# Kernel optimization log

Hardware: AMD Instinct MI355X
Metric: run time of the kernel (lower is better)

Reference implementation:

```python
import jax, jax.numpy as jnp
import numpy as np

N_NODES = 100000
N_EDGES = 1200000
IN_F = 64
OUT_F = 64


def setup_inputs() -> dict:
    key = jax.random.key(0)
    ks = jax.random.split(key, 8)
    rows = jax.random.randint(ks[0], (N_EDGES,), 0, N_NODES)
    cols = jax.random.randint(ks[1], (N_EDGES,), 0, N_NODES)
    vals = jax.random.uniform(ks[2], (N_EDGES,), dtype=jnp.float32)
    features = jax.random.normal(ks[3], (N_NODES, IN_F), dtype=jnp.float32)
    W1 = jax.random.normal(ks[4], (IN_F, OUT_F), dtype=jnp.float32) / np.sqrt(IN_F)
    b1 = jax.random.normal(ks[5], (OUT_F,), dtype=jnp.float32) * 0.01
    W2 = jax.random.normal(ks[6], (IN_F, OUT_F), dtype=jnp.float32) / np.sqrt(IN_F)
    b2 = jax.random.normal(ks[7], (OUT_F,), dtype=jnp.float32) * 0.01
    return {"rows": rows, "cols": cols, "vals": vals, "features": features,
            "W1": W1, "b1": b1, "W2": W2, "b2": b2}


def _spmm(rows, cols, vals, x):
    # y[r] = sum_{e: rows[e]==r} vals[e] * x[cols[e]]  -- COO SpMM via gather + segment_sum
    msgs = vals[:, None] * x[cols]  # [E, F]
    return jax.ops.segment_sum(msgs, rows, num_segments=N_NODES)


def reference(rows, cols, vals, features, W1, b1, W2, b2):
    # L1 = laplacian + selfLoop(identity)  =>  L1 @ X = L @ X + X
    agg1 = _spmm(rows, cols, vals, features) + features          # [N, inF]
    inter_feature = features * features                           # elementwise square
    agg2 = _spmm(rows, cols, vals, inter_feature)                 # [N, inF]
    part1 = agg1 @ W1 + b1                                        # linear
    part2 = agg2 @ W2 + b2                                        # interActTransform
    return part1 + part2
```

## Files before the change

kernel.cpp:

```cpp
#include <hip/hip_runtime.h>


#define ROWS_PER_BUCKET 128
#define ROW_SHIFT 7
#define NBUCK_PAD 784
#define SCAN_T 196
#define CAP 2048
#define CHUNK 4096
#define MAXB 2048
#define COL_BITS 17
#define COL_MASK 0x1FFFF
#define OVF_CAP 65536

typedef __attribute__((ext_vector_type(8))) short bf16x8;
typedef __attribute__((ext_vector_type(4))) float f32x4;

__device__ __forceinline__ unsigned short f2bf(float x) {
    unsigned u = __float_as_uint(x);
    unsigned r = (u + 0x7FFFu + ((u >> 16) & 1u)) >> 16;
    return (unsigned short)r;
}
__device__ __forceinline__ float bf2f(unsigned short h) {
    return __uint_as_float(((unsigned)h) << 16);
}

__global__ __launch_bounds__(256) void node_transform(
    const float* __restrict__ X, const float* __restrict__ W1,
    const float* __restrict__ b1, const float* __restrict__ W2,
    const float* __restrict__ b2, unsigned short* __restrict__ Yb,
    float* __restrict__ Z, int n_nodes)
{
    const int tid = threadIdx.x;
    const int lane = tid & 63;
    const int wave = tid >> 6;
    const int lg = lane >> 4;
    const int lr = lane & 15;

    const int base = blockIdx.x * 128 + wave * 32;

    bf16x8 bw1[2][4];
    bf16x8 bw2[2][4];
#pragma unroll
    for (int ks = 0; ks < 2; ++ks) {
#pragma unroll
        for (int cf = 0; cf < 4; ++cf) {
            const int col = cf * 16 + lr;
            const int k0 = ks * 32 + lg * 8;
            bf16x8 t1, t2;
#pragma unroll
            for (int j = 0; j < 8; ++j) {
                t1[j] = (short)f2bf(W1[(k0 + j) * 64 + col]);
                t2[j] = (short)f2bf(W2[(k0 + j) * 64 + col]);
            }
            bw1[ks][cf] = t1;
            bw2[ks][cf] = t2;
        }
    }

    f32x4 acc1[2][4];
    f32x4 acc2[2][4];
#pragma unroll
    for (int rf = 0; rf < 2; ++rf)
#pragma unroll
        for (int cf = 0; cf < 4; ++cf) {
            acc1[rf][cf] = (f32x4){0.f, 0.f, 0.f, 0.f};
            acc2[rf][cf] = (f32x4){0.f, 0.f, 0.f, 0.f};
        }

#pragma unroll
    for (int rf = 0; rf < 2; ++rf) {
        const int row = base + rf * 16 + lr;
        const bool rok = row < n_nodes;
        const float* xp = X + (size_t)row * 64 + lg * 8;
#pragma unroll
        for (int ks = 0; ks < 2; ++ks) {
            float xv[8];
            if (rok) {
                float4 v0 = *(const float4*)(xp + ks * 32);
                float4 v1 = *(const float4*)(xp + ks * 32 + 4);
                xv[0] = v0.x; xv[1] = v0.y; xv[2] = v0.z; xv[3] = v0.w;
                xv[4] = v1.x; xv[5] = v1.y; xv[6] = v1.z; xv[7] = v1.w;
            } else {
#pragma unroll
                for (int j = 0; j < 8; ++j) xv[j] = 0.f;
            }
            bf16x8 a, q;
#pragma unroll
            for (int j = 0; j < 8; ++j) {
                a[j] = (short)f2bf(xv[j]);
                float s = xv[j] * xv[j];
                q[j] = (short)f2bf(s);
            }
#pragma unroll
            for (int cf = 0; cf < 4; ++cf) {
                acc1[rf][cf] = __builtin_amdgcn_mfma_f32_16x16x32_bf16(
                    a, bw1[ks][cf], acc1[rf][cf], 0, 0, 0);
                acc2[rf][cf] = __builtin_amdgcn_mfma_f32_16x16x32_bf16(
                    q, bw2[ks][cf], acc2[rf][cf], 0, 0, 0);
            }
        }
    }

    float bsv[4];
#pragma unroll
    for (int cf = 0; cf < 4; ++cf)
        bsv[cf] = b1[cf * 16 + lr] + b2[cf * 16 + lr];

#pragma unroll
    for (int rf = 0; rf < 2; ++rf) {
#pragma unroll
        for (int i = 0; i < 4; ++i) {
            const int row = base + rf * 16 + lg * 4 + i;
            if (row < n_nodes) {
#pragma unroll
                for (int cf = 0; cf < 4; ++cf) {
                    const float v1 = acc1[rf][cf][i];
                    const float y = v1 + acc2[rf][cf][i];
                    const float z = v1 + bsv[cf];
                    Yb[(size_t)row * 64 + cf * 16 + lr] = f2bf(y);
                    Z[(size_t)row * 64 + cf * 16 + lr] = z;
                }
            }
        }
    }
}


__global__ __launch_bounds__(256) void cursor_init(
    int* __restrict__ gcursor, int* __restrict__ ovf_count, int nbp) {
    int i = blockIdx.x * 256 + threadIdx.x;
    if (i < nbp) gcursor[i] = i * CAP;
    if (i == 0) *ovf_count = 0;
}

__global__ __launch_bounds__(256) void bin_scatter(
    const int* __restrict__ rows, const int* __restrict__ cols,
    const float* __restrict__ vals, int* __restrict__ gcursor,
    int2* __restrict__ packed, int* __restrict__ ovf_count,
    int4* __restrict__ ovf, int n_edges) {
    __shared__ int lcount[NBUCK_PAD];
    __shared__ int lstart[NBUCK_PAD];
    __shared__ int lcursor[NBUCK_PAD];
    __shared__ int gbase[NBUCK_PAD];
    __shared__ int sx[CHUNK];
    __shared__ int sy[CHUNK];
    __shared__ unsigned short sbk[CHUNK];

    int tid = threadIdx.x;
    int eb0 = blockIdx.x * CHUNK;
    int cnt = min(CHUNK, n_edges - eb0);

    for (int k = tid; k < NBUCK_PAD; k += 256) lcount[k] = 0;
    __syncthreads();

    for (int i = tid; i < cnt; i += 256)
        atomicAdd(&lcount[rows[eb0 + i] >> ROW_SHIFT], 1);
    __syncthreads();

    int c0 = 0, c1 = 0, c2 = 0, c3 = 0, psum = 0;
    if (tid < SCAN_T) {
        c0 = lcount[tid * 4 + 0]; c1 = lcount[tid * 4 + 1];
        c2 = lcount[tid * 4 + 2]; c3 = lcount[tid * 4 + 3];
        psum = c0 + c1 + c2 + c3;
    }
    sx[tid] = psum;
    __syncthreads();
#pragma unroll
    for (int o = 1; o < 256; o <<= 1) {
        int t = (tid >= o) ? sx[tid - o] : 0;
        __syncthreads();
        sx[tid] += t;
        __syncthreads();
    }
    int base0 = sx[tid] - psum;
    __syncthreads();
    if (tid < SCAN_T) {
        lstart[tid * 4 + 0] = base0;
        lstart[tid * 4 + 1] = base0 + c0;
        lstart[tid * 4 + 2] = base0 + c0 + c1;
        lstart[tid * 4 + 3] = base0 + c0 + c1 + c2;
    }
    __syncthreads();

    for (int k = tid; k < NBUCK_PAD; k += 256) {
        lcursor[k] = lstart[k];
        if (lcount[k] > 0) gbase[k] = atomicAdd(&gcursor[k], lcount[k]);
    }
    __syncthreads();

    for (int i = tid; i < cnt; i += 256) {
        int r = rows[eb0 + i];
        int b = r >> ROW_SHIFT;
        int p = atomicAdd(&lcursor[b], 1);
        sx[p] = ((r & (ROWS_PER_BUCKET - 1)) << COL_BITS) | cols[eb0 + i];
        sy[p] = __float_as_int(vals[eb0 + i]);
        sbk[p] = (unsigned short)b;
    }
    __syncthreads();

    for (int i = tid; i < cnt; i += 256) {
        int b = sbk[i];
        int dest = gbase[b] + (i - lstart[b]);
        if (dest < (b + 1) * CAP) {
            packed[dest] = make_int2(sx[i], sy[i]);
        } else {
            int p = atomicAdd(ovf_count, 1);
            if (p < OVF_CAP)
                ovf[p] = make_int4(b * ROWS_PER_BUCKET + (sx[i] >> COL_BITS),
                                   sx[i] & COL_MASK, sy[i], 0);
        }
    }
}

__global__ __launch_bounds__(256) void bucket_gather_rows(
    const int* __restrict__ gcursor, const int2* __restrict__ packed,
    const unsigned short* __restrict__ Yb, float* __restrict__ out,
    int n_nodes) {
    __shared__ int2 sxy[MAXB];
    __shared__ int hist[ROWS_PER_BUCKET];
    __shared__ int chs[ROWS_PER_BUCKET];
    __shared__ int chc[ROWS_PER_BUCKET];

    int tid = threadIdx.x;
    int bucket = blockIdx.x >> 1;
    int rhalf = (blockIdx.x & 1) * 64;
    int fpair = tid & 31;
    int rowlane = tid >> 5;
    int s = bucket * CAP;
    int e = min(gcursor[bucket], s + CAP);
    int row0 = bucket * ROWS_PER_BUCKET;
    const unsigned* __restrict__ Y32 = (const unsigned*)Yb;

    for (int cb = s; cb < e; cb += MAXB) {
        int cnt = min(MAXB, e - cb);

        if (tid < ROWS_PER_BUCKET) hist[tid] = 0;
        __syncthreads();

        for (int i = tid; i < cnt; i += 256)
            atomicAdd(&hist[packed[cb + i].x >> COL_BITS], 1);
        __syncthreads();

        if (tid < ROWS_PER_BUCKET) chs[tid] = hist[tid];
        __syncthreads();
#pragma unroll
        for (int o = 1; o < ROWS_PER_BUCKET; o <<= 1) {
            int t = 0;
            if (tid < ROWS_PER_BUCKET && tid >= o) t = chs[tid - o];
            __syncthreads();
            if (tid < ROWS_PER_BUCKET) chs[tid] += t;
            __syncthreads();
        }
        if (tid < ROWS_PER_BUCKET) {
            int excl = chs[tid] - hist[tid];
            chs[tid] = excl;
            chc[tid] = excl;
        }
        __syncthreads();

        for (int i = tid; i < cnt; i += 256) {
            int2 a = packed[cb + i];
            int p = atomicAdd(&chc[a.x >> COL_BITS], 1);
            sxy[p] = a;
        }
        __syncthreads();

        for (int rr = 0; rr < 8; ++rr) {
            int r = rhalf + rowlane * 8 + rr;
            int rc = hist[r];
            int node = row0 + r;
            if (rc == 0 || node >= n_nodes) continue;
            int rs = chs[r];
            float a0 = 0.f, a1 = 0.f;
            int j = 0;
            for (; j + 8 <= rc; j += 8) {
                int2 e0 = sxy[rs + j + 0], e1 = sxy[rs + j + 1];
                int2 e2 = sxy[rs + j + 2], e3 = sxy[rs + j + 3];
                int2 e4 = sxy[rs + j + 4], e5 = sxy[rs + j + 5];
                int2 e6 = sxy[rs + j + 6], e7 = sxy[rs + j + 7];
                unsigned u0 = Y32[(size_t)(e0.x & COL_MASK) * 32 + fpair];
                unsigned u1 = Y32[(size_t)(e1.x & COL_MASK) * 32 + fpair];
                unsigned u2 = Y32[(size_t)(e2.x & COL_MASK) * 32 + fpair];
                unsigned u3 = Y32[(size_t)(e3.x & COL_MASK) * 32 + fpair];
                unsigned u4 = Y32[(size_t)(e4.x & COL_MASK) * 32 + fpair];
                unsigned u5 = Y32[(size_t)(e5.x & COL_MASK) * 32 + fpair];
                unsigned u6 = Y32[(size_t)(e6.x & COL_MASK) * 32 + fpair];
                unsigned u7 = Y32[(size_t)(e7.x & COL_MASK) * 32 + fpair];
                float v0 = __int_as_float(e0.y), v1 = __int_as_float(e1.y);
                float v2 = __int_as_float(e2.y), v3 = __int_as_float(e3.y);
                float v4 = __int_as_float(e4.y), v5 = __int_as_float(e5.y);
                float v6 = __int_as_float(e6.y), v7 = __int_as_float(e7.y);
                a0 = fmaf(v0, __uint_as_float(u0 << 16), a0);
                a1 = fmaf(v0, __uint_as_float(u0 & 0xFFFF0000u), a1);
                a0 = fmaf(v1, __uint_as_float(u1 << 16), a0);
                a1 = fmaf(v1, __uint_as_float(u1 & 0xFFFF0000u), a1);
                a0 = fmaf(v2, __uint_as_float(u2 << 16), a0);
                a1 = fmaf(v2, __uint_as_float(u2 & 0xFFFF0000u), a1);
                a0 = fmaf(v3, __uint_as_float(u3 << 16), a0);
                a1 = fmaf(v3, __uint_as_float(u3 & 0xFFFF0000u), a1);
                a0 = fmaf(v4, __uint_as_float(u4 << 16), a0);
                a1 = fmaf(v4, __uint_as_float(u4 & 0xFFFF0000u), a1);
                a0 = fmaf(v5, __uint_as_float(u5 << 16), a0);
                a1 = fmaf(v5, __uint_as_float(u5 & 0xFFFF0000u), a1);
                a0 = fmaf(v6, __uint_as_float(u6 << 16), a0);
                a1 = fmaf(v6, __uint_as_float(u6 & 0xFFFF0000u), a1);
                a0 = fmaf(v7, __uint_as_float(u7 << 16), a0);
                a1 = fmaf(v7, __uint_as_float(u7 & 0xFFFF0000u), a1);
            }
            for (; j + 2 <= rc; j += 2) {
                int2 e0 = sxy[rs + j + 0], e1 = sxy[rs + j + 1];
                unsigned u0 = Y32[(size_t)(e0.x & COL_MASK) * 32 + fpair];
                unsigned u1 = Y32[(size_t)(e1.x & COL_MASK) * 32 + fpair];
                float v0 = __int_as_float(e0.y), v1 = __int_as_float(e1.y);
                a0 = fmaf(v0, __uint_as_float(u0 << 16), a0);
                a1 = fmaf(v0, __uint_as_float(u0 & 0xFFFF0000u), a1);
                a0 = fmaf(v1, __uint_as_float(u1 << 16), a0);
                a1 = fmaf(v1, __uint_as_float(u1 & 0xFFFF0000u), a1);
            }
            if (j < rc) {
                int2 e0 = sxy[rs + j];
                unsigned u0 = Y32[(size_t)(e0.x & COL_MASK) * 32 + fpair];
                float v0 = __int_as_float(e0.y);
                a0 = fmaf(v0, __uint_as_float(u0 << 16), a0);
                a1 = fmaf(v0, __uint_as_float(u0 & 0xFFFF0000u), a1);
            }
            float2* op = (float2*)(out + (size_t)node * 64 + fpair * 2);
            float2 o = *op;
            o.x += a0; o.y += a1;
            *op = o;
        }
        __syncthreads();
    }
}

__global__ __launch_bounds__(256) void overflow_scatter(
    const int* __restrict__ ovf_count, const int4* __restrict__ ovf,
    const unsigned short* __restrict__ Yb, float* __restrict__ out) {
    int cnt = min(*ovf_count, OVF_CAP);
    long long total = (long long)cnt * 64;
    for (long long i = blockIdx.x * 256 + threadIdx.x; i < total;
         i += (long long)gridDim.x * 256) {
        int e = (int)(i >> 6), f = (int)(i & 63);
        int4 a = ovf[e];
        atomicAdd(&out[(size_t)a.x * 64 + f],
                  __int_as_float(a.z) * bf2f(Yb[(size_t)a.y * 64 + f]));
    }
}


__global__ __launch_bounds__(256) void edge_scatter(
    const int* __restrict__ rows, const int* __restrict__ cols,
    const float* __restrict__ vals, const unsigned short* __restrict__ Yb,
    float* __restrict__ out, int n_edges)
{
    int t = blockIdx.x * 256 + threadIdx.x;
    int e = t >> 4;
    int f = (t & 15) << 2;
    if (e >= n_edges) return;
    int r = rows[e];
    int c = cols[e];
    float v = vals[e];
    const unsigned short* y = Yb + (size_t)c * 64 + f;
    float* o = out + (size_t)r * 64 + f;
    atomicAdd(o + 0, v * bf2f(y[0]));
    atomicAdd(o + 1, v * bf2f(y[1]));
    atomicAdd(o + 2, v * bf2f(y[2]));
    atomicAdd(o + 3, v * bf2f(y[3]));
}

extern "C" void kernel_launch(void* const* d_in, const int* in_sizes, int n_in,
                              void* d_out, int out_size, void* d_ws, size_t ws_size,
                              hipStream_t stream) {
    const int*   rows = (const int*)d_in[0];
    const int*   cols = (const int*)d_in[1];
    const float* vals = (const float*)d_in[2];
    const float* X    = (const float*)d_in[3];
    const float* W1   = (const float*)d_in[4];
    const float* b1   = (const float*)d_in[5];
    const float* W2   = (const float*)d_in[6];
    const float* b2   = (const float*)d_in[7];
    float* out = (float*)d_out;

    const int n_edges = in_sizes[0];
    const int n_nodes = in_sizes[3] / 64;
    const int nbuck = (n_nodes + ROWS_PER_BUCKET - 1) / ROWS_PER_BUCKET;

    char* ws = (char*)d_ws;
    size_t o_Yb     = 0;
    size_t o_packed = o_Yb + (size_t)n_nodes * 64 * 2;
    size_t o_ovf    = o_packed + (size_t)NBUCK_PAD * CAP * 8;
    size_t o_gcurs  = o_ovf + (size_t)OVF_CAP * 16;
    size_t o_ovfcnt = o_gcurs + NBUCK_PAD * 4;
    size_t need     = o_ovfcnt + 16;

    unsigned short* Yb = (unsigned short*)(ws + o_Yb);

    int nblocks = (n_nodes + 127) / 128;
    node_transform<<<nblocks, 256, 0, stream>>>(X, W1, b1, W2, b2, Yb, out, n_nodes);

    if (ws_size >= need && nbuck <= NBUCK_PAD && n_nodes <= (1 << COL_BITS)) {
        int2* packed  = (int2*)(ws + o_packed);
        int4* ovf     = (int4*)(ws + o_ovf);
        int*  gcursor = (int*)(ws + o_gcurs);
        int*  ovfcnt  = (int*)(ws + o_ovfcnt);

        int eb = (n_edges + CHUNK - 1) / CHUNK;

        cursor_init<<<(NBUCK_PAD + 255) / 256, 256, 0, stream>>>(gcursor, ovfcnt, NBUCK_PAD);
        bin_scatter<<<eb, 256, 0, stream>>>(rows, cols, vals, gcursor, packed,
                                            ovfcnt, ovf, n_edges);
        bucket_gather_rows<<<nbuck * 2, 256, 0, stream>>>(gcursor, packed, Yb, out, n_nodes);
        overflow_scatter<<<128, 256, 0, stream>>>(ovfcnt, ovf, Yb, out);
    } else {
        long long threads = (long long)n_edges * 16;
        int eblocks = (int)((threads + 255) / 256);
        edge_scatter<<<eblocks, 256, 0, stream>>>(rows, cols, vals, Yb, out, n_edges);
    }
}
```

Baseline: 172.4 us.

## Replace per-row sort with shared-memory atomic accumulation in bucket kernel; fold cursor init

The bucket gather kernel no longer builds a per-row histogram, prefix scan and counting sort in shared memory. Each block now owns a whole bucket of 128 rows, loads edges in chunks of 1024 and accumulates gathered contributions into a padded 128x66 shared-memory float accumulator with LDS atomics, then adds the tile to the output with float4 writes. This removes the scan barriers and sort work but uses LDS float atomics, which can contend, and halves the grid size. The separate cursor_init launch is folded into node_transform to save one kernel launch.

```diff
diff --git a/kernel.cpp b/kernel.cpp
--- a/kernel.cpp
+++ b/kernel.cpp
@@ -7,7 +7,7 @@
 #define SCAN_T 196
 #define CAP 2048
 #define CHUNK 4096
-#define MAXB 2048
+#define SEDGE 1024
 #define COL_BITS 17
 #define COL_MASK 0x1FFFF
 #define OVF_CAP 65536
@@ -28,9 +28,17 @@
     const float* __restrict__ X, const float* __restrict__ W1,
     const float* __restrict__ b1, const float* __restrict__ W2,
     const float* __restrict__ b2, unsigned short* __restrict__ Yb,
-    float* __restrict__ Z, int n_nodes)
+    float* __restrict__ Z, int n_nodes,
+    int* __restrict__ gcursor, int* __restrict__ ovf_count)
 {
     const int tid = threadIdx.x;
+
+    if (gcursor) {
+        int gi = blockIdx.x * 256 + tid;
+        if (gi < NBUCK_PAD) gcursor[gi] = gi * CAP;
+        if (gi == 0) *ovf_count = 0;
+    }
+
     const int lane = tid & 63;
     const int wave = tid >> 6;
     const int lg = lane >> 4;
@@ -125,13 +133,6 @@
     }
 }
 
-
-__global__ __launch_bounds__(256) void cursor_init(
-    int* __restrict__ gcursor, int* __restrict__ ovf_count, int nbp) {
-    int i = blockIdx.x * 256 + threadIdx.x;
-    if (i < nbp) gcursor[i] = i * CAP;
-    if (i == 0) *ovf_count = 0;
-}
 
 __global__ __launch_bounds__(256) void bin_scatter(
     const int* __restrict__ rows, const int* __restrict__ cols,
@@ -212,124 +213,75 @@
     }
 }
 
-__global__ __launch_bounds__(256) void bucket_gather_rows(
+__global__ __launch_bounds__(256) void bucket_accum(
     const int* __restrict__ gcursor, const int2* __restrict__ packed,
     const unsigned short* __restrict__ Yb, float* __restrict__ out,
     int n_nodes) {
-    __shared__ int2 sxy[MAXB];
-    __shared__ int hist[ROWS_PER_BUCKET];
-    __shared__ int chs[ROWS_PER_BUCKET];
-    __shared__ int chc[ROWS_PER_BUCKET];
+    __shared__ float acc[ROWS_PER_BUCKET][66];
+    __shared__ int2 sed[SEDGE];
 
     int tid = threadIdx.x;
-    int bucket = blockIdx.x >> 1;
-    int rhalf = (blockIdx.x & 1) * 64;
+    int bucket = blockIdx.x;
     int fpair = tid & 31;
-    int rowlane = tid >> 5;
+    int hw = tid >> 5;
     int s = bucket * CAP;
     int e = min(gcursor[bucket], s + CAP);
     int row0 = bucket * ROWS_PER_BUCKET;
     const unsigned* __restrict__ Y32 = (const unsigned*)Yb;
 
-    for (int cb = s; cb < e; cb += MAXB) {
-        int cnt = min(MAXB, e - cb);
-
-        if (tid < ROWS_PER_BUCKET) hist[tid] = 0;
+    for (int i = tid; i < ROWS_PER_BUCKET * 66; i += 256)
+        ((float*)acc)[i] = 0.f;
+    __syncthreads();
+
+    for (int cb = s; cb < e; cb += SEDGE) {
+        int cnt = min(SEDGE, e - cb);
+        for (int i = tid; i < cnt; i += 256)
+            sed[i] = packed[cb + i];
         __syncthreads();
 
-        for (int i = tid; i < cnt; i += 256)
-            atomicAdd(&hist[packed[cb + i].x >> COL_BITS], 1);
+        int i = hw;
+        for (; i + 24 < cnt; i += 32) {
+            int2 e0 = sed[i], e1 = sed[i + 8], e2 = sed[i + 16], e3 = sed[i + 24];
+            unsigned u0 = Y32[(size_t)(e0.x & COL_MASK) * 32 + fpair];
+            unsigned u1 = Y32[(size_t)(e1.x & COL_MASK) * 32 + fpair];
+            unsigned u2 = Y32[(size_t)(e2.x & COL_MASK) * 32 + fpair];
+            unsigned u3 = Y32[(size_t)(e3.x & COL_MASK) * 32 + fpair];
+            float v0 = __int_as_float(e0.y), v1 = __int_as_float(e1.y);
+            float v2 = __int_as_float(e2.y), v3 = __int_as_float(e3.y);
+            int r0 = e0.x >> COL_BITS, r1 = e1.x >> COL_BITS;
+            int r2 = e2.x >> COL_BITS, r3 = e3.x >> COL_BITS;
+            atomicAdd(&acc[r0][2 * fpair],     v0 * __uint_as_float(u0 << 16));
+            atomicAdd(&acc[r0][2 * fpair + 1], v0 * __uint_as_float(u0 & 0xFFFF0000u));
+            atomicAdd(&acc[r1][2 * fpair],     v1 * __uint_as_float(u1 << 16));
+            atomicAdd(&acc[r1][2 * fpair + 1], v1 * __uint_as_float(u1 & 0xFFFF0000u));
+            atomicAdd(&acc[r2][2 * fpair],     v2 * __uint_as_float(u2 << 16));
+            atomicAdd(&acc[r2][2 * fpair + 1], v2 * __uint_as_float(u2 & 0xFFFF0000u));
+            atomicAdd(&acc[r3][2 * fpair],     v3 * __uint_as_float(u3 << 16));
+            atomicAdd(&acc[r3][2 * fpair + 1], v3 * __uint_as_float(u3 & 0xFFFF0000u));
+        }
+        for (; i < cnt; i += 8) {
+            int2 e0 = sed[i];
+            unsigned u0 = Y32[(size_t)(e0.x & COL_MASK) * 32 + fpair];
+            float v0 = __int_as_float(e0.y);
+            int r0 = e0.x >> COL_BITS;
+            atomicAdd(&acc[r0][2 * fpair],     v0 * __uint_as_float(u0 << 16));
+            atomicAdd(&acc[r0][2 * fpair + 1], v0 * __uint_as_float(u0 & 0xFFFF0000u));
+        }
         __syncthreads();
-
-        if (tid < ROWS_PER_BUCKET) chs[tid] = hist[tid];
-        __syncthreads();
-#pragma unroll
-        for (int o = 1; o < ROWS_PER_BUCKET; o <<= 1) {
-            int t = 0;
-            if (tid < ROWS_PER_BUCKET && tid >= o) t = chs[tid - o];
-            __syncthreads();
-            if (tid < ROWS_PER_BUCKET) chs[tid] += t;
-            __syncthreads();
-        }
-        if (tid < ROWS_PER_BUCKET) {
-            int excl = chs[tid] - hist[tid];
-            chs[tid] = excl;
-            chc[tid] = excl;
-        }
-        __syncthreads();
-
-        for (int i = tid; i < cnt; i += 256) {
-            int2 a = packed[cb + i];
-            int p = atomicAdd(&chc[a.x >> COL_BITS], 1);
-            sxy[p] = a;
-        }
-        __syncthreads();
-
-        for (int rr = 0; rr < 8; ++rr) {
-            int r = rhalf + rowlane * 8 + rr;
-            int rc = hist[r];
-            int node = row0 + r;
-            if (rc == 0 || node >= n_nodes) continue;
-            int rs = chs[r];
-            float a0 = 0.f, a1 = 0.f;
-            int j = 0;
-            for (; j + 8 <= rc; j += 8) {
-                int2 e0 = sxy[rs + j + 0], e1 = sxy[rs + j + 1];
-                int2 e2 = sxy[rs + j + 2], e3 = sxy[rs + j + 3];
-                int2 e4 = sxy[rs + j + 4], e5 = sxy[rs + j + 5];
-                int2 e6 = sxy[rs + j + 6], e7 = sxy[rs + j + 7];
-                unsigned u0 = Y32[(size_t)(e0.x & COL_MASK) * 32 + fpair];
-                unsigned u1 = Y32[(size_t)(e1.x & COL_MASK) * 32 + fpair];
-                unsigned u2 = Y32[(size_t)(e2.x & COL_MASK) * 32 + fpair];
-                unsigned u3 = Y32[(size_t)(e3.x & COL_MASK) * 32 + fpair];
-                unsigned u4 = Y32[(size_t)(e4.x & COL_MASK) * 32 + fpair];
-                unsigned u5 = Y32[(size_t)(e5.x & COL_MASK) * 32 + fpair];
-                unsigned u6 = Y32[(size_t)(e6.x & COL_MASK) * 32 + fpair];
-                unsigned u7 = Y32[(size_t)(e7.x & COL_MASK) * 32 + fpair];
-                float v0 = __int_as_float(e0.y), v1 = __int_as_float(e1.y);
-                float v2 = __int_as_float(e2.y), v3 = __int_as_float(e3.y);
-                float v4 = __int_as_float(e4.y), v5 = __int_as_float(e5.y);
-                float v6 = __int_as_float(e6.y), v7 = __int_as_float(e7.y);
-                a0 = fmaf(v0, __uint_as_float(u0 << 16), a0);
-                a1 = fmaf(v0, __uint_as_float(u0 & 0xFFFF0000u), a1);
-                a0 = fmaf(v1, __uint_as_float(u1 << 16), a0);
-                a1 = fmaf(v1, __uint_as_float(u1 & 0xFFFF0000u), a1);
-                a0 = fmaf(v2, __uint_as_float(u2 << 16), a0);
-                a1 = fmaf(v2, __uint_as_float(u2 & 0xFFFF0000u), a1);
-                a0 = fmaf(v3, __uint_as_float(u3 << 16), a0);
-                a1 = fmaf(v3, __uint_as_float(u3 & 0xFFFF0000u), a1);
-                a0 = fmaf(v4, __uint_as_float(u4 << 16), a0);
-                a1 = fmaf(v4, __uint_as_float(u4 & 0xFFFF0000u), a1);
-                a0 = fmaf(v5, __uint_as_float(u5 << 16), a0);
-                a1 = fmaf(v5, __uint_as_float(u5 & 0xFFFF0000u), a1);
-                a0 = fmaf(v6, __uint_as_float(u6 << 16), a0);
-                a1 = fmaf(v6, __uint_as_float(u6 & 0xFFFF0000u), a1);
-                a0 = fmaf(v7, __uint_as_float(u7 << 16), a0);
-                a1 = fmaf(v7, __uint_as_float(u7 & 0xFFFF0000u), a1);
-            }
-            for (; j + 2 <= rc; j += 2) {
-                int2 e0 = sxy[rs + j + 0], e1 = sxy[rs + j + 1];
-                unsigned u0 = Y32[(size_t)(e0.x & COL_MASK) * 32 + fpair];
-                unsigned u1 = Y32[(size_t)(e1.x & COL_MASK) * 32 + fpair];
-                float v0 = __int_as_float(e0.y), v1 = __int_as_float(e1.y);
-                a0 = fmaf(v0, __uint_as_float(u0 << 16), a0);
-                a1 = fmaf(v0, __uint_as_float(u0 & 0xFFFF0000u), a1);
-                a0 = fmaf(v1, __uint_as_float(u1 << 16), a0);
-                a1 = fmaf(v1, __uint_as_float(u1 & 0xFFFF0000u), a1);
-            }
-            if (j < rc) {
-                int2 e0 = sxy[rs + j];
-                unsigned u0 = Y32[(size_t)(e0.x & COL_MASK) * 32 + fpair];
-                float v0 = __int_as_float(e0.y);
-                a0 = fmaf(v0, __uint_as_float(u0 << 16), a0);
-                a1 = fmaf(v0, __uint_as_float(u0 & 0xFFFF0000u), a1);
-            }
-            float2* op = (float2*)(out + (size_t)node * 64 + fpair * 2);
-            float2 o = *op;
-            o.x += a0; o.y += a1;
+    }
+
+    for (int idx = tid; idx < ROWS_PER_BUCKET * 16; idx += 256) {
+        int r = idx >> 4, q = (idx & 15) * 4;
+        int node = row0 + r;
+        if (node < n_nodes) {
+            float4* op = (float4*)(out + (size_t)node * 64 + q);
+            float4 o = *op;
+            o.x += acc[r][q + 0];
+            o.y += acc[r][q + 1];
+            o.z += acc[r][q + 2];
+            o.w += acc[r][q + 3];
             *op = o;
         }
-        __syncthreads();
     }
 }
 
@@ -395,21 +347,23 @@
 
     unsigned short* Yb = (unsigned short*)(ws + o_Yb);
 
+    const bool fastpath =
+        ws_size >= need && nbuck <= NBUCK_PAD && n_nodes <= (1 << COL_BITS);
+
+    int2* packed  = (int2*)(ws + o_packed);
+    int4* ovf     = (int4*)(ws + o_ovf);
+    int*  gcursor = fastpath ? (int*)(ws + o_gcurs) : (int*)0;
+    int*  ovfcnt  = (int*)(ws + o_ovfcnt);
+
     int nblocks = (n_nodes + 127) / 128;
-    node_transform<<<nblocks, 256, 0, stream>>>(X, W1, b1, W2, b2, Yb, out, n_nodes);
-
-    if (ws_size >= need && nbuck <= NBUCK_PAD && n_nodes <= (1 << COL_BITS)) {
-        int2* packed  = (int2*)(ws + o_packed);
-        int4* ovf     = (int4*)(ws + o_ovf);
-        int*  gcursor = (int*)(ws + o_gcurs);
-        int*  ovfcnt  = (int*)(ws + o_ovfcnt);
-
+    node_transform<<<nblocks, 256, 0, stream>>>(X, W1, b1, W2, b2, Yb, out,
+                                                n_nodes, gcursor, ovfcnt);
+
+    if (fastpath) {
         int eb = (n_edges + CHUNK - 1) / CHUNK;
-
-        cursor_init<<<(NBUCK_PAD + 255) / 256, 256, 0, stream>>>(gcursor, ovfcnt, NBUCK_PAD);
         bin_scatter<<<eb, 256, 0, stream>>>(rows, cols, vals, gcursor, packed,
                                             ovfcnt, ovf, n_edges);
-        bucket_gather_rows<<<nbuck * 2, 256, 0, stream>>>(gcursor, packed, Yb, out, n_nodes);
+        bucket_accum<<<nbuck, 256, 0, stream>>>(gcursor, packed, Yb, out, n_nodes);
         overflow_scatter<<<128, 256, 0, stream>>>(ovfcnt, ovf, Yb, out);
     } else {
         long long threads = (long long)n_edges * 16;
```

Measured after the change: 655.6 us. +280.4%, slower.
